# Kernel tuning notes

Hardware: AMD Instinct MI355X
Metric: run time of the kernel (lower is better)

## Reference

```python
import jax, jax.numpy as jnp
import numpy as np

N = 30000
NUM_FEAT = 129   # data.x.shape[1] + 1
NUM_CLASSES = 40
HID = 64

def _gat_conv(x, src, dst, W, a_src, a_dst, bias):
    """PyG GATConv (concat=True, negative_slope=0.2), self-loops pre-added to src/dst."""
    n = x.shape[0]
    H, C = a_src.shape
    h = (x @ W).reshape(n, H, C)                       # [N,H,C]
    alpha_s = jnp.sum(h * a_src[None], axis=-1)        # [N,H]
    alpha_d = jnp.sum(h * a_dst[None], axis=-1)        # [N,H]
    e = jax.nn.leaky_relu(alpha_s[src] + alpha_d[dst], 0.2)   # [E,H]
    m = jax.ops.segment_max(e, dst, num_segments=n)
    m = jnp.where(jnp.isfinite(m), m, 0.0)
    ex = jnp.exp(e - m[dst])
    denom = jax.ops.segment_sum(ex, dst, num_segments=n)
    alpha = ex / (denom[dst] + 1e-16)                  # segment softmax over in-edges
    out = jax.ops.segment_sum(h[src] * alpha[:, :, None], dst, num_segments=n)
    return out.reshape(n, H * C) + bias


def setup_inputs() -> dict:
    key = jax.random.key(0)
    ks = jax.random.split(key, 16)
    E = 480000
    x = jax.random.normal(ks[0], (N, NUM_FEAT), dtype=jnp.float32)
    edge_index = jax.random.randint(ks[1], (2, E), 0, N, dtype=jnp.int64)
    def w(k, shape, fan_in):
        return (jax.random.normal(k, shape, dtype=jnp.float32) * (1.0 / np.sqrt(fan_in))).astype(jnp.float32)
    # conv1: in=129, H=7, C=64
    W1 = w(ks[2], (NUM_FEAT, 7 * HID), NUM_FEAT)
    a1s = w(ks[3], (7, HID), HID); a1d = w(ks[4], (7, HID), HID)
    b1 = jnp.zeros((7 * HID,), jnp.float32)
    # conv2: in=448, H=6, C=64
    W2 = w(ks[5], (7 * HID, 6 * HID), 7 * HID)
    a2s = w(ks[6], (6, HID), HID); a2d = w(ks[7], (6, HID), HID)
    b2 = jnp.zeros((6 * HID,), jnp.float32)
    # conv3: in=384, H=6, C=40
    W3 = w(ks[8], (6 * HID, 6 * NUM_CLASSES), 6 * HID)
    a3s = w(ks[9], (6, NUM_CLASSES), NUM_CLASSES); a3d = w(ks[10], (6, NUM_CLASSES), NUM_CLASSES)
    b3 = jnp.zeros((6 * NUM_CLASSES,), jnp.float32)
    return {"x": x, "edge_index": edge_index,
            "W1": W1, "a1s": a1s, "a1d": a1d, "b1": b1,
            "W2": W2, "a2s": a2s, "a2d": a2d, "b2": b2,
            "W3": W3, "a3s": a3s, "a3d": a3d, "b3": b3}


def reference(x, edge_index, W1, a1s, a1d, b1, W2, a2s, a2d, b2, W3, a3s, a3d, b3):
    n = x.shape[0]
    loop = jnp.arange(n, dtype=edge_index.dtype)
    src = jnp.concatenate([edge_index[0], loop])   # PyG add_self_loops=True
    dst = jnp.concatenate([edge_index[1], loop])
    # dropout is identity in eval mode
    h = _gat_conv(x, src, dst, W1, a1s, a1d, b1)
    h = jax.nn.relu(h)
    h = _gat_conv(h, src, dst, W2, a2s, a2d, b2)
    h = jax.nn.relu(h)
    out = _gat_conv(h, src, dst, W3, a3s, a3d, b3)
    return out
```

## Files before the change

kernel.cpp:

```cpp
#include <hip/hip_runtime.h>
#include <hip/hip_bf16.h>


#define NFEAT 129
#define MPAD  30080

typedef __attribute__((ext_vector_type(8))) short short8v;
typedef __attribute__((ext_vector_type(8))) unsigned short u16x8;
typedef __attribute__((ext_vector_type(8))) __bf16 bf16x8;
typedef __attribute__((ext_vector_type(4))) float f32x4;
typedef unsigned short u16;

union FragU { short8v s; bf16x8 b; };

__device__ inline u16 f2bf(float x) {
    unsigned u = __builtin_bit_cast(unsigned, x);
    unsigned r = (u + 0x7fffu + ((u >> 16) & 1u)) >> 16;
    return (u16)r;
}
__device__ inline float bf2f(u16 b) {
    unsigned u = ((unsigned)b) << 16;
    return __builtin_bit_cast(float, u);
}
__device__ inline float h2f(u16 u) { return (float)__builtin_bit_cast(_Float16, u); }
__device__ inline u16 f2h(float v) { return __builtin_bit_cast(u16, (_Float16)v); }


__global__ __launch_bounds__(256) void init_cnt_k(int* __restrict__ cnt, int n) {
    int i = blockIdx.x * 256 + threadIdx.x;
    if (i < n) cnt[i] = 1;
}

__global__ __launch_bounds__(256) void hist_k(const int* __restrict__ dst, int* __restrict__ cnt, int E) {
    int e = blockIdx.x * 256 + threadIdx.x;
    if (e < E) atomicAdd(&cnt[dst[e]], 1);
}

__global__ __launch_bounds__(1024) void scan_k(const int* __restrict__ cnt, int* __restrict__ row_ptr, int n) {
    __shared__ int part[1024];
    int tid = threadIdx.x;
    int per = (n + 1023) >> 10;
    int base = tid * per;
    int s = 0;
    for (int j = 0; j < per; ++j) {
        int idx = base + j;
        if (idx < n) s += cnt[idx];
    }
    part[tid] = s;
    __syncthreads();
    for (int off = 1; off < 1024; off <<= 1) {
        int v = 0;
        if (tid >= off) v = part[tid - off];
        __syncthreads();
        if (tid >= off) part[tid] += v;
        __syncthreads();
    }
    int run = (tid > 0) ? part[tid - 1] : 0;
    for (int j = 0; j < per; ++j) {
        int idx = base + j;
        if (idx < n) { row_ptr[idx] = run; run += cnt[idx]; }
    }
    if (tid == 0) row_ptr[n] = part[1023];
}

__global__ __launch_bounds__(256) void scatter_k(const int* __restrict__ src, const int* __restrict__ dst,
                                                 const int* __restrict__ row_ptr, int* __restrict__ fill,
                                                 int* __restrict__ col, int E, int n) {
    int e = blockIdx.x * 256 + threadIdx.x;
    if (e < E + n) {
        int s, d;
        if (e < E) { s = src[e]; d = dst[e]; }
        else       { s = d = e - E; }
        int pos = row_ptr[d] + atomicAdd(&fill[d], 1);
        col[pos] = s;
    }
}


__global__ __launch_bounds__(256) void xsplit_k(const float* __restrict__ in,
                                                u16* __restrict__ hi, u16* __restrict__ lo,
                                                int Nn, int K, int Kp, int Mp) {
    int idx = blockIdx.x * 256 + threadIdx.x;
    if (idx >= Mp * Kp) return;
    int m = idx / Kp, k = idx - m * Kp;
    float v = (m < Nn && k < K) ? in[(size_t)m * K + k] : 0.f;
    u16 h = f2bf(v);
    hi[idx] = h;
    lo[idx] = f2bf(v - bf2f(h));
}


__global__ __launch_bounds__(256) void wsplitAll_k(const float* __restrict__ W1,
                                                   const float* __restrict__ W2,
                                                   const float* __restrict__ W3,
                                                   u16* __restrict__ hi, u16* __restrict__ lo) {
    int idx = blockIdx.x * 256 + threadIdx.x;
    if (idx >= 352256) return;
    const float* W; int loc, Kp, K, N;
    if (idx < 81920)       { W = W1; loc = idx;          Kp = 160; K = 129; N = 448; }
    else if (idx < 253952) { W = W2; loc = idx - 81920;  Kp = 448; K = 448; N = 384; }
    else                   { W = W3; loc = idx - 253952; Kp = 384; K = 384; N = 240; }
    int nn = loc / Kp, k = loc - nn * Kp;
    float v = (k < K && nn < N) ? W[(size_t)k * N + nn] : 0.f;
    u16 h = f2bf(v);
    hi[idx] = h;
    lo[idx] = f2bf(v - bf2f(h));
}


__global__ __launch_bounds__(256) void projAll_k(
    const float* __restrict__ W1, const float* __restrict__ a1s, const float* __restrict__ a1d,
    const float* __restrict__ W2, const float* __restrict__ a2s, const float* __restrict__ a2d,
    const float* __restrict__ W3, const float* __restrict__ a3s, const float* __restrict__ a3d,
    float* __restrict__ Ps, float* __restrict__ Pd) {
    int idx = blockIdx.x * 256 + threadIdx.x;
    if (idx >= 992 * 8) return;
    int row = idx >> 3, h = idx & 7;
    const float *W, *as_, *ad_; int k, K, Ncols, H, C;
    if (row < 160)      { k = row;       K = 129; W = W1; as_ = a1s; ad_ = a1d; Ncols = 448; H = 7; C = 64; }
    else if (row < 608) { k = row - 160; K = 448; W = W2; as_ = a2s; ad_ = a2d; Ncols = 384; H = 6; C = 64; }
    else                { k = row - 608; K = 384; W = W3; as_ = a3s; ad_ = a3d; Ncols = 240; H = 6; C = 40; }
    float ps = 0.f, pd = 0.f;
    if (h < H && k < K) {
        const float* wr = W + (size_t)k * Ncols + h * C;
        const float* ar = as_ + h * C;
        const float* dr = ad_ + h * C;
        for (int c = 0; c < C; ++c) {
            float wv = wr[c];
            ps += wv * ar[c];
            pd += wv * dr[c];
        }
    }
    Ps[idx] = ps;
    Pd[idx] = pd;
}


__global__ __launch_bounds__(256) void zeropads_k(u16* __restrict__ h1hi, u16* __restrict__ h1lo,
                                                  int Nn) {
    int tot = (MPAD - Nn) * 448;
    int idx = blockIdx.x * 256 + threadIdx.x;
    if (idx < tot) {
        h1hi[(size_t)Nn * 448 + idx] = 0;
        h1lo[(size_t)Nn * 448 + idx] = 0;
    }
}


__global__ __launch_bounds__(256) void alpha1_k(const float* __restrict__ x,
                                                const float* __restrict__ Ps,
                                                const float* __restrict__ Pd,
                                                float* __restrict__ oS, float* __restrict__ oD, int n) {
    int wv = threadIdx.x >> 6, lane = threadIdx.x & 63;
    int i = blockIdx.x * 4 + wv;
    if (i >= n) return;
    const float* row = x + (size_t)i * NFEAT;
    float x0 = row[lane], x1 = row[64 + lane];
    float ps[8], pd[8];
    #pragma unroll
    for (int h = 0; h < 8; ++h) {
        ps[h] = x0 * Ps[lane * 8 + h] + x1 * Ps[(64 + lane) * 8 + h];
        pd[h] = x0 * Pd[lane * 8 + h] + x1 * Pd[(64 + lane) * 8 + h];
    }
    if (lane == 0) {
        float x2 = row[128];
        #pragma unroll
        for (int h = 0; h < 8; ++h) {
            ps[h] += x2 * Ps[128 * 8 + h];
            pd[h] += x2 * Pd[128 * 8 + h];
        }
    }
    #pragma unroll
    for (int h = 0; h < 8; ++h) {
        #pragma unroll
        for (int off = 32; off; off >>= 1) {
            ps[h] += __shfl_xor(ps[h], off);
            pd[h] += __shfl_xor(pd[h], off);
        }
    }
    if (lane == 0) {
        #pragma unroll
        for (int h = 0; h < 8; ++h) {
            oS[(size_t)i * 8 + h] = ps[h];
            oD[(size_t)i * 8 + h] = pd[h];
        }
    }
}


__device__ __forceinline__ int swz(int r, int s) {
    return (r << 2) | ((s ^ (r & 3) ^ ((r >> 2) & 3)) & 3);
}


__global__ __launch_bounds__(256) void gemm16(
    const u16* __restrict__ Ahi, const u16* __restrict__ Alo,
    const u16* __restrict__ Bhi, const u16* __restrict__ Blo,
    u16* __restrict__ C16, int M, int Ncols, int Kp)
{
    __shared__ __align__(16) u16 sAh[128 * 32];
    __shared__ __align__(16) u16 sAl[128 * 32];
    __shared__ __align__(16) u16 sBh[128 * 32];
    __shared__ __align__(16) u16 sBl[128 * 32];
    const int tid = threadIdx.x;
    const int m0 = blockIdx.y * 128;
    const int n0 = blockIdx.x * 128;
    const int lane = tid & 63, wave = tid >> 6;
    const int wm = wave >> 1, wn = wave & 1;
    const int l15 = lane & 15, lg = lane >> 4;
    const int r0 = tid >> 2, s0 = tid & 3;
    const int w0 = swz(r0, s0), w1 = swz(r0 + 64, s0);
    f32x4 acc[4][4] = {};

    for (int k0 = 0; k0 < Kp; k0 += 32) {
        size_t gA0 = (size_t)(m0 + r0) * Kp + k0 + s0 * 8;
        size_t gA1 = (size_t)(m0 + r0 + 64) * Kp + k0 + s0 * 8;
        size_t gB0 = (size_t)(n0 + r0) * Kp + k0 + s0 * 8;
        size_t gB1 = (size_t)(n0 + r0 + 64) * Kp + k0 + s0 * 8;
        short8v ah0 = *(const short8v*)(Ahi + gA0);
        short8v ah1 = *(const short8v*)(Ahi + gA1);
        short8v al0 = *(const short8v*)(Alo + gA0);
        short8v al1 = *(const short8v*)(Alo + gA1);
        short8v bh0 = *(const short8v*)(Bhi + gB0);
        short8v bh1 = *(const short8v*)(Bhi + gB1);
        short8v bl0 = *(const short8v*)(Blo + gB0);
        short8v bl1 = *(const short8v*)(Blo + gB1);
        __syncthreads();
        ((short8v*)sAh)[w0] = ah0; ((short8v*)sAh)[w1] = ah1;
        ((short8v*)sAl)[w0] = al0; ((short8v*)sAl)[w1] = al1;
        ((short8v*)sBh)[w0] = bh0; ((short8v*)sBh)[w1] = bh1;
        ((short8v*)sBl)[w0] = bl0; ((short8v*)sBl)[w1] = bl1;
        __syncthreads();
        FragU fah[4], fal[4], fbh[4], fbl[4];
        #pragma unroll
        for (int mf = 0; mf < 4; ++mf) {
            int rr = wm * 64 + mf * 16 + l15;
            int idx = swz(rr, lg);
            fah[mf].s = ((const short8v*)sAh)[idx];
            fal[mf].s = ((const short8v*)sAl)[idx];
        }
        #pragma unroll
        for (int nf = 0; nf < 4; ++nf) {
            int rr = wn * 64 + nf * 16 + l15;
            int idx = swz(rr, lg);
            fbh[nf].s = ((const short8v*)sBh)[idx];
            fbl[nf].s = ((const short8v*)sBl)[idx];
        }
        #pragma unroll
        for (int mf = 0; mf < 4; ++mf) {
            #pragma unroll
            for (int nf = 0; nf < 4; ++nf) {
                acc[mf][nf] = __builtin_amdgcn_mfma_f32_16x16x32_bf16(fah[mf].b, fbh[nf].b, acc[mf][nf], 0, 0, 0);
                acc[mf][nf] = __builtin_amdgcn_mfma_f32_16x16x32_bf16(fah[mf].b, fbl[nf].b, acc[mf][nf], 0, 0, 0);
                acc[mf][nf] = __builtin_amdgcn_mfma_f32_16x16x32_bf16(fal[mf].b, fbh[nf].b, acc[mf][nf], 0, 0, 0);
            }
        }
    }
    #pragma unroll
    for (int mf = 0; mf < 4; ++mf) {
        #pragma unroll
        for (int nf = 0; nf < 4; ++nf) {
            int colg = n0 + wn * 64 + nf * 16 + l15;
            if (colg >= Ncols) continue;
            #pragma unroll
            for (int r = 0; r < 4; ++r) {
                int rowg = m0 + wm * 64 + mf * 16 + lg * 4 + r;
                if (rowg < M) C16[(size_t)rowg * Ncols + colg] = f2h(acc[mf][nf][r]);
            }
        }
    }
}


template <int H, int C, bool RELU, bool SPLIT, bool PROJ>
__global__ __launch_bounds__(256) void aggF_k(
    const u16* __restrict__ hf,
    const float* __restrict__ as_, const float* __restrict__ ad_,
    const float* __restrict__ bias,
    const int* __restrict__ row_ptr, const int* __restrict__ col,
    const float* __restrict__ Pns, const float* __restrict__ Pnd,
    float* __restrict__ nas, float* __restrict__ nad,
    float* __restrict__ outf, u16* __restrict__ ohi, u16* __restrict__ olo,
    int n)
{
    constexpr int HC = H * C;
    constexpr int LACT = HC / 8;
    const int wv = threadIdx.x >> 6, lane = threadIdx.x & 63;
    const int i = blockIdx.x * 4 + wv;
    if (i >= n) return;
    const int ch0 = lane * 8;
    const bool act = lane < LACT;
    const int h = act ? (ch0 / C) : 0;
    const bool lead = act && ((ch0 % C) == 0);
    const int beg = row_ptr[i], end = row_ptr[i + 1];
    float acc[8] = {};
    float dp = 0.f;
    if (act) {
        const float adh = ad_[(size_t)i * 8 + h];
        int e = beg;
        for (; e + 4 <= end; e += 4) {
            int sA = col[e],     sB = col[e + 1];
            int sC = col[e + 2], sD = col[e + 3];
            float fA = as_[(size_t)sA * 8 + h] + adh;
            float fB = as_[(size_t)sB * 8 + h] + adh;
            float fC = as_[(size_t)sC * 8 + h] + adh;
            float fD = as_[(size_t)sD * 8 + h] + adh;
            u16x8 vA = *(const u16x8*)(hf + (size_t)sA * HC + ch0);
            u16x8 vB = *(const u16x8*)(hf + (size_t)sB * HC + ch0);
            u16x8 vC = *(const u16x8*)(hf + (size_t)sC * HC + ch0);
            u16x8 vD = *(const u16x8*)(hf + (size_t)sD * HC + ch0);
            fA = fA > 0.f ? fA : 0.2f * fA;
            fB = fB > 0.f ? fB : 0.2f * fB;
            fC = fC > 0.f ? fC : 0.2f * fC;
            fD = fD > 0.f ? fD : 0.2f * fD;
            float wA = __expf(fA), wB = __expf(fB);
            float wC = __expf(fC), wD = __expf(fD);
            #pragma unroll
            for (int j = 0; j < 8; ++j)
                acc[j] += wA * h2f(vA[j]) + wB * h2f(vB[j])
                        + wC * h2f(vC[j]) + wD * h2f(vD[j]);
            if (lead) dp += (wA + wB) + (wC + wD);
        }
        for (; e + 2 <= end; e += 2) {
            int sA = col[e], sB = col[e + 1];
            float fA = as_[(size_t)sA * 8 + h] + adh;
            float fB = as_[(size_t)sB * 8 + h] + adh;
            u16x8 vA = *(const u16x8*)(hf + (size_t)sA * HC + ch0);
            u16x8 vB = *(const u16x8*)(hf + (size_t)sB * HC + ch0);
            fA = fA > 0.f ? fA : 0.2f * fA;
            fB = fB > 0.f ? fB : 0.2f * fB;
            float wA = __expf(fA), wB = __expf(fB);
            #pragma unroll
            for (int j = 0; j < 8; ++j)
                acc[j] += wA * h2f(vA[j]) + wB * h2f(vB[j]);
            if (lead) dp += wA + wB;
        }
        if (e < end) {
            int sA = col[e];
            float fA = as_[(size_t)sA * 8 + h] + adh;
            u16x8 vA = *(const u16x8*)(hf + (size_t)sA * HC + ch0);
            fA = fA > 0.f ? fA : 0.2f * fA;
            float wA = __expf(fA);
            #pragma unroll
            for (int j = 0; j < 8; ++j)
                acc[j] += wA * h2f(vA[j]);
            if (lead) dp += wA;
        }
    }
    const float den = __shfl(dp, h * (C / 8)) + 1e-16f;
    float o[8];
    #pragma unroll
    for (int j = 0; j < 8; ++j) o[j] = 0.f;
    if (act) {
        #pragma unroll
        for (int j = 0; j < 8; ++j) {
            float v = acc[j] / den + bias[ch0 + j];
            if (RELU) v = fmaxf(v, 0.f);
            o[j] = v;
        }
        size_t base = (size_t)i * HC + ch0;
        if constexpr (SPLIT) {
            u16x8 ph, pl;
            #pragma unroll
            for (int j = 0; j < 8; ++j) {
                u16 hi = f2bf(o[j]);
                ph[j] = hi;
                pl[j] = f2bf(o[j] - bf2f(hi));
            }
            *(u16x8*)(ohi + base) = ph;
            *(u16x8*)(olo + base) = pl;
        } else {
            float4 q0; q0.x = o[0]; q0.y = o[1]; q0.z = o[2]; q0.w = o[3];
            float4 q1; q1.x = o[4]; q1.y = o[5]; q1.z = o[6]; q1.w = o[7];
            *(float4*)(outf + base) = q0;
            *(float4*)(outf + base + 4) = q1;
        }
    }
    if constexpr (PROJ) {
        float ps[8] = {}, pd[8] = {};
        if (act) {
            #pragma unroll
            for (int j = 0; j < 8; ++j) {
                const float* prs = Pns + (size_t)(ch0 + j) * 8;
                const float* prd = Pnd + (size_t)(ch0 + j) * 8;
                #pragma unroll
                for (int hp = 0; hp < 8; ++hp) {
                    ps[hp] += o[j] * prs[hp];
                    pd[hp] += o[j] * prd[hp];
                }
            }
        }
        #pragma unroll
        for (int hp = 0; hp < 8; ++hp) {
            #pragma unroll
            for (int off = 32; off; off >>= 1) {
                ps[hp] += __shfl_xor(ps[hp], off);
                pd[hp] += __shfl_xor(pd[hp], off);
            }
        }
        if (lane == 0) {
            #pragma unroll
            for (int hp = 0; hp < 8; ++hp) {
                nas[(size_t)i * 8 + hp] = ps[hp];
                nad[(size_t)i * 8 + hp] = pd[hp];
            }
        }
    }
}


extern "C" void kernel_launch(void* const* d_in, const int* in_sizes, int n_in,
                              void* d_out, int out_size, void* d_ws, size_t ws_size,
                              hipStream_t stream) {
    const float* x   = (const float*)d_in[0];
    const int*   ei  = (const int*)d_in[1];
    const float* W1  = (const float*)d_in[2];
    const float* a1s = (const float*)d_in[3];
    const float* a1d = (const float*)d_in[4];
    const float* b1  = (const float*)d_in[5];
    const float* W2  = (const float*)d_in[6];
    const float* a2s = (const float*)d_in[7];
    const float* a2d = (const float*)d_in[8];
    const float* b2  = (const float*)d_in[9];
    const float* W3  = (const float*)d_in[10];
    const float* a3s = (const float*)d_in[11];
    const float* a3d = (const float*)d_in[12];
    const float* b3  = (const float*)d_in[13];
    float* out = (float*)d_out;

    const int Nn = in_sizes[0] / NFEAT;
    const int E  = in_sizes[1] / 2;
    const int Et = E + Nn;
    const int* srcp = ei;
    const int* dstp = ei + E;

    char* ws = (char*)d_ws;
    size_t off = 0;
    auto carve = [&](size_t bytes) -> char* {
        char* p = ws + off;
        off += (bytes + 255) & ~(size_t)255;
        return p;
    };
    u16*   hbuf16 = (u16*)carve((size_t)MPAD * 448 * 2);
    u16*   h1hi  = (u16*)carve((size_t)MPAD * 448 * 2);
    u16*   h1lo  = (u16*)carve((size_t)MPAD * 448 * 2);
    u16*   Xhi   = (u16*)carve((size_t)MPAD * 160 * 2);
    u16*   Xlo   = (u16*)carve((size_t)MPAD * 160 * 2);
    u16*   Wthi  = (u16*)carve((size_t)352256 * 2);
    u16*   Wtlo  = (u16*)carve((size_t)352256 * 2);
    int*   col   = (int*)carve((size_t)Et * 4);
    int* row_ptr = (int*)carve((size_t)(Nn + 1) * 4);
    int*   cnt   = (int*)carve((size_t)Nn * 4);
    float* aA    = (float*)carve((size_t)Nn * 8 * 4);
    float* dA    = (float*)carve((size_t)Nn * 8 * 4);
    float* aB    = (float*)carve((size_t)Nn * 8 * 4);
    float* dB    = (float*)carve((size_t)Nn * 8 * 4);
    float* Ps    = (float*)carve((size_t)992 * 8 * 4);
    float* Pd    = (float*)carve((size_t)992 * 8 * 4);
    (void)ws_size;

    const int nb4 = (Nn + 3) / 4;
    const int mg  = MPAD / 128;

    init_cnt_k<<<(Nn + 255) / 256, 256, 0, stream>>>(cnt, Nn);
    hist_k<<<(E + 255) / 256, 256, 0, stream>>>(dstp, cnt, E);
    scan_k<<<1, 1024, 0, stream>>>(cnt, row_ptr, Nn);
    hipMemsetAsync(cnt, 0, (size_t)Nn * 4, stream);
    scatter_k<<<(Et + 255) / 256, 256, 0, stream>>>(srcp, dstp, row_ptr, cnt, col, E, Nn);

    xsplit_k<<<((MPAD * 160) + 255) / 256, 256, 0, stream>>>(x, Xhi, Xlo, Nn, NFEAT, 160, MPAD);
    wsplitAll_k<<<(352256 + 255) / 256, 256, 0, stream>>>(W1, W2, W3, Wthi, Wtlo);
    projAll_k<<<(992 * 8 + 255) / 256, 256, 0, stream>>>(W1, a1s, a1d, W2, a2s, a2d, W3, a3s, a3d, Ps, Pd);
    zeropads_k<<<(((MPAD - Nn) * 448) + 255) / 256, 256, 0, stream>>>(h1hi, h1lo, Nn);

    alpha1_k<<<nb4, 256, 0, stream>>>(x, Ps, Pd, aA, dA, Nn);
    gemm16<<<dim3(4, mg), 256, 0, stream>>>(Xhi, Xlo, Wthi, Wtlo, hbuf16, Nn, 448, 160);
    aggF_k<7, 64, true, true, true><<<nb4, 256, 0, stream>>>(
        hbuf16, aA, dA, b1, row_ptr, col, Ps + 1280, Pd + 1280, aB, dB,
        nullptr, h1hi, h1lo, Nn);

    gemm16<<<dim3(3, mg), 256, 0, stream>>>(h1hi, h1lo, Wthi + 81920, Wtlo + 81920, hbuf16, Nn, 384, 448);
    aggF_k<6, 64, true, true, true><<<nb4, 256, 0, stream>>>(
        hbuf16, aB, dB, b2, row_ptr, col, Ps + 4864, Pd + 4864, aA, dA,
        nullptr, h1hi, h1lo, Nn);

    gemm16<<<dim3(2, mg), 256, 0, stream>>>(h1hi, h1lo, Wthi + 253952, Wtlo + 253952, hbuf16, Nn, 240, 384);
    aggF_k<6, 40, false, false, false><<<nb4, 256, 0, stream>>>(
        hbuf16, aA, dA, b3, row_ptr, col, nullptr, nullptr, nullptr, nullptr,
        out, nullptr, nullptr, Nn);
}
```

Baseline: 588.8 us.

## Split GAT aggregation channels across two blocks with partial alpha projections

```diff
diff --git a/kernel.cpp b/kernel.cpp
--- a/kernel.cpp
+++ b/kernel.cpp
@@ -196,7 +196,7 @@
 __global__ __launch_bounds__(256) void gemm16(
     const u16* __restrict__ Ahi, const u16* __restrict__ Alo,
     const u16* __restrict__ Bhi, const u16* __restrict__ Blo,
-    u16* __restrict__ C16, int M, int Ncols, int Kp)
+    u16* __restrict__ C16, int M, int Ncols, int Kp, int ldc)
 {
     __shared__ __align__(16) u16 sAh[128 * 32];
     __shared__ __align__(16) u16 sAl[128 * 32];
@@ -265,31 +265,31 @@
             #pragma unroll
             for (int r = 0; r < 4; ++r) {
                 int rowg = m0 + wm * 64 + mf * 16 + lg * 4 + r;
-                if (rowg < M) C16[(size_t)rowg * Ncols + colg] = f2h(acc[mf][nf][r]);
-            }
-        }
-    }
-}
-
-
-template <int H, int C, bool RELU, bool SPLIT, bool PROJ>
-__global__ __launch_bounds__(256) void aggF_k(
-    const u16* __restrict__ hf,
+                if (rowg < M) C16[(size_t)rowg * ldc + colg] = f2h(acc[mf][nf][r]);
+            }
+        }
+    }
+}
+
+
+template <int H, int C, int CPB, bool RELU, bool SPLIT, bool PROJ>
+__global__ __launch_bounds__(256) void aggH_k(
+    const u16* __restrict__ hf, int ldh,
     const float* __restrict__ as_, const float* __restrict__ ad_,
     const float* __restrict__ bias,
     const int* __restrict__ row_ptr, const int* __restrict__ col,
     const float* __restrict__ Pns, const float* __restrict__ Pnd,
-    float* __restrict__ nas, float* __restrict__ nad,
+    float* __restrict__ nasP, float* __restrict__ nadP,
     float* __restrict__ outf, u16* __restrict__ ohi, u16* __restrict__ olo,
     int n)
 {
     constexpr int HC = H * C;
-    constexpr int LACT = HC / 8;
     const int wv = threadIdx.x >> 6, lane = threadIdx.x & 63;
     const int i = blockIdx.x * 4 + wv;
     if (i >= n) return;
-    const int ch0 = lane * 8;
-    const bool act = lane < LACT;
+    const int cb = blockIdx.y * CPB;
+    const int ch0 = cb + lane * 8;
+    const bool act = (lane * 8 < CPB) && (ch0 < HC);
     const int h = act ? (ch0 / C) : 0;
     const bool lead = act && ((ch0 % C) == 0);
     const int beg = row_ptr[i], end = row_ptr[i + 1];
@@ -305,10 +305,10 @@
             float fB = as_[(size_t)sB * 8 + h] + adh;
             float fC = as_[(size_t)sC * 8 + h] + adh;
             float fD = as_[(size_t)sD * 8 + h] + adh;
-            u16x8 vA = *(const u16x8*)(hf + (size_t)sA * HC + ch0);
-            u16x8 vB = *(const u16x8*)(hf + (size_t)sB * HC + ch0);
-            u16x8 vC = *(const u16x8*)(hf + (size_t)sC * HC + ch0);
-            u16x8 vD = *(const u16x8*)(hf + (size_t)sD * HC + ch0);
+            u16x8 vA = *(const u16x8*)(hf + (size_t)sA * ldh + ch0);
+            u16x8 vB = *(const u16x8*)(hf + (size_t)sB * ldh + ch0);
+            u16x8 vC = *(const u16x8*)(hf + (size_t)sC * ldh + ch0);
+            u16x8 vD = *(const u16x8*)(hf + (size_t)sD * ldh + ch0);
             fA = fA > 0.f ? fA : 0.2f * fA;
             fB = fB > 0.f ? fB : 0.2f * fB;
             fC = fC > 0.f ? fC : 0.2f * fC;
@@ -321,24 +321,10 @@
                         + wC * h2f(vC[j]) + wD * h2f(vD[j]);
             if (lead) dp += (wA + wB) + (wC + wD);
         }
-        for (; e + 2 <= end; e += 2) {
-            int sA = col[e], sB = col[e + 1];
-            float fA = as_[(size_t)sA * 8 + h] + adh;
-            float fB = as_[(size_t)sB * 8 + h] + adh;
-            u16x8 vA = *(const u16x8*)(hf + (size_t)sA * HC + ch0);
-            u16x8 vB = *(const u16x8*)(hf + (size_t)sB * HC + ch0);
-            fA = fA > 0.f ? fA : 0.2f * fA;
-            fB = fB > 0.f ? fB : 0.2f * fB;
-            float wA = __expf(fA), wB = __expf(fB);
-            #pragma unroll
-            for (int j = 0; j < 8; ++j)
-                acc[j] += wA * h2f(vA[j]) + wB * h2f(vB[j]);
-            if (lead) dp += wA + wB;
-        }
-        if (e < end) {
+        for (; e < end; ++e) {
             int sA = col[e];
             float fA = as_[(size_t)sA * 8 + h] + adh;
-            u16x8 vA = *(const u16x8*)(hf + (size_t)sA * HC + ch0);
+            u16x8 vA = *(const u16x8*)(hf + (size_t)sA * ldh + ch0);
             fA = fA > 0.f ? fA : 0.2f * fA;
             float wA = __expf(fA);
             #pragma unroll
@@ -347,7 +333,8 @@
             if (lead) dp += wA;
         }
     }
-    const float den = __shfl(dp, h * (C / 8)) + 1e-16f;
+    const int li = act ? ((h * C - cb) >> 3) : 0;
+    const float den = __shfl(dp, li) + 1e-16f;
     float o[8];
     #pragma unroll
     for (int j = 0; j < 8; ++j) o[j] = 0.f;
@@ -399,12 +386,25 @@
             }
         }
         if (lane == 0) {
+            size_t pb = (size_t)blockIdx.y * n * 8 + (size_t)i * 8;
             #pragma unroll
             for (int hp = 0; hp < 8; ++hp) {
-                nas[(size_t)i * 8 + hp] = ps[hp];
-                nad[(size_t)i * 8 + hp] = pd[hp];
-            }
-        }
+                nasP[pb + hp] = ps[hp];
+                nadP[pb + hp] = pd[hp];
+            }
+        }
+    }
+}
+
+
+__global__ __launch_bounds__(256) void comb_k(const float* __restrict__ aP,
+                                              const float* __restrict__ dP,
+                                              float* __restrict__ ao,
+                                              float* __restrict__ dov, int n8) {
+    int idx = blockIdx.x * 256 + threadIdx.x;
+    if (idx < n8) {
+        ao[idx]  = aP[idx] + aP[n8 + idx];
+        dov[idx] = dP[idx] + dP[n8 + idx];
     }
 }
 
@@ -441,7 +441,7 @@
         off += (bytes + 255) & ~(size_t)255;
         return p;
     };
-    u16*   hbuf16 = (u16*)carve((size_t)MPAD * 448 * 2);
+    u16*   hbuf16 = (u16*)carve((size_t)MPAD * 512 * 2);
     u16*   h1hi  = (u16*)carve((size_t)MPAD * 448 * 2);
     u16*   h1lo  = (u16*)carve((size_t)MPAD * 448 * 2);
     u16*   Xhi   = (u16*)carve((size_t)MPAD * 160 * 2);
@@ -455,12 +455,15 @@
     float* dA    = (float*)carve((size_t)Nn * 8 * 4);
     float* aB    = (float*)carve((size_t)Nn * 8 * 4);
     float* dB    = (float*)carve((size_t)Nn * 8 * 4);
+    float* nasP  = (float*)carve((size_t)2 * Nn * 8 * 4);
+    float* nadP  = (float*)carve((size_t)2 * Nn * 8 * 4);
     float* Ps    = (float*)carve((size_t)992 * 8 * 4);
     float* Pd    = (float*)carve((size_t)992 * 8 * 4);
     (void)ws_size;
 
     const int nb4 = (Nn + 3) / 4;
     const int mg  = MPAD / 128;
+    const int n8  = Nn * 8;
 
     init_cnt_k<<<(Nn + 255) / 256, 256, 0, stream>>>(cnt, Nn);
     hist_k<<<(E + 255) / 256, 256, 0, stream>>>(dstp, cnt, E);
@@ -474,18 +477,20 @@
     zeropads_k<<<(((MPAD - Nn) * 448) + 255) / 256, 256, 0, stream>>>(h1hi, h1lo, Nn);
 
     alpha1_k<<<nb4, 256, 0, stream>>>(x, Ps, Pd, aA, dA, Nn);
-    gemm16<<<dim3(4, mg), 256, 0, stream>>>(Xhi, Xlo, Wthi, Wtlo, hbuf16, Nn, 448, 160);
-    aggF_k<7, 64, true, true, true><<<nb4, 256, 0, stream>>>(
-        hbuf16, aA, dA, b1, row_ptr, col, Ps + 1280, Pd + 1280, aB, dB,
+    gemm16<<<dim3(4, mg), 256, 0, stream>>>(Xhi, Xlo, Wthi, Wtlo, hbuf16, Nn, 448, 160, 512);
+    aggH_k<7, 64, 256, true, true, true><<<dim3(nb4, 2), 256, 0, stream>>>(
+        hbuf16, 512, aA, dA, b1, row_ptr, col, Ps + 1280, Pd + 1280, nasP, nadP,
         nullptr, h1hi, h1lo, Nn);
-
-    gemm16<<<dim3(3, mg), 256, 0, stream>>>(h1hi, h1lo, Wthi + 81920, Wtlo + 81920, hbuf16, Nn, 384, 448);
-    aggF_k<6, 64, true, true, true><<<nb4, 256, 0, stream>>>(
-        hbuf16, aB, dB, b2, row_ptr, col, Ps + 4864, Pd + 4864, aA, dA,
+    comb_k<<<(n8 + 255) / 256, 256, 0, stream>>>(nasP, nadP, aB, dB, n8);
+
+    gemm16<<<dim3(3, mg), 256, 0, stream>>>(h1hi, h1lo, Wthi + 81920, Wtlo + 81920, hbuf16, Nn, 384, 448, 384);
+    aggH_k<6, 64, 192, true, true, true><<<dim3(nb4, 2), 256, 0, stream>>>(
+        hbuf16, 384, aB, dB, b2, row_ptr, col, Ps + 4864, Pd + 4864, nasP, nadP,
         nullptr, h1hi, h1lo, Nn);
-
-    gemm16<<<dim3(2, mg), 256, 0, stream>>>(h1hi, h1lo, Wthi + 253952, Wtlo + 253952, hbuf16, Nn, 240, 384);
-    aggF_k<6, 40, false, false, false><<<nb4, 256, 0, stream>>>(
-        hbuf16, aA, dA, b3, row_ptr, col, nullptr, nullptr, nullptr, nullptr,
+    comb_k<<<(n8 + 255) / 256, 256, 0, stream>>>(nasP, nadP, aA, dA, n8);
+
+    gemm16<<<dim3(2, mg), 256, 0, stream>>>(h1hi, h1lo, Wthi + 253952, Wtlo + 253952, hbuf16, Nn, 240, 384, 256);
+    aggH_k<6, 40, 240, false, false, false><<<dim3(nb4, 1), 256, 0, stream>>>(
+        hbuf16, 256, aA, dA, b3, row_ptr, col, nullptr, nullptr, nullptr, nullptr,
         out, nullptr, nullptr, Nn);
 }
```

After: 669.7 us. 13.7% more time.
